# Kernel tuning notes

Hardware: AMD Instinct MI355X
Metric: run time of the kernel (lower is better)

The kernel has to match this reference:

```python
import jax, jax.numpy as jnp
import numpy as np

EPS = 1e-5
C = 128
B = 16384
SYMBIOTIC = 4.0
NUM_PARENTS = 16
CHILDREN_PER_PARENT = 7


def _inverse(v):
    # torch: sort -> rank -> reversed rank -> gather sorted values
    idx0 = np.argsort(v, kind='stable')
    value = v[idx0]
    idx1 = np.argsort(idx0, kind='stable')  # ranks
    idx2 = v.shape[0] - 1 - idx1
    return value[idx2]


def _build_stats():
    counts = np.floor(50000.0 * 0.97 ** np.arange(C)) + 1.0  # long-tailed
    N = counts.sum()
    weight = (N / counts).astype(np.float32)
    prior = np.eye(C, dtype=np.float32)
    for p in range(NUM_PARENTS):
        ch = NUM_PARENTS + CHILDREN_PER_PARENT * p + np.arange(CHILDREN_PER_PARENT)
        prior[p, ch] = 1.0
    prior_me = (prior == 0).astype(np.float32)          # 1 - prior, keep only exact 1s
    prior_ms = prior - np.eye(C, dtype=np.float32)      # prior (0/1) minus eye
    v1_sig = np.log(N / counts - 1.0 + EPS).astype(np.float32)
    v2_sig = _inverse(v1_sig).astype(np.float32)
    v1_sm = np.log(counts / N + EPS).astype(np.float32)
    v2_sm = _inverse(v1_sm).astype(np.float32)
    return weight, prior_me, prior_ms, v1_sig, v2_sig, v1_sm, v2_sm


def setup_inputs() -> dict:
    key = jax.random.key(0)
    k1, k2 = jax.random.split(key)
    weight, prior_me, prior_ms, v1s, v2s, v1m, v2m = _build_stats()
    logits = 0.5 * jax.random.normal(k1, (12, B, C), dtype=jnp.float32)
    target = (jax.random.uniform(k2, (B, C)) < 0.1).astype(jnp.float32)
    return {
        'logits': logits, 'target': target,
        'weight': jnp.asarray(weight),
        'prior_me': jnp.asarray(prior_me), 'prior_ms': jnp.asarray(prior_ms),
        'v1_sigmoid': jnp.asarray(v1s), 'v2_sigmoid': jnp.asarray(v2s),
        'v1_softmax': jnp.asarray(v1m), 'v2_softmax': jnp.asarray(v2m),
    }


def reference(logits, target, weight, prior_me, prior_ms,
              v1_sigmoid, v2_sigmoid, v1_softmax, v2_softmax):
    zero = jnp.zeros_like(v1_sigmoid)
    # experts 0-5: sigmoid variants (long-tailed / balanced / inversed, twice)
    sig_shift = jnp.stack([zero, v1_sigmoid, v1_sigmoid - v2_sigmoid] * 2)  # [6,C]
    a_sig = jax.nn.sigmoid(logits[:6] - sig_shift[:, None, :])
    # experts 6-11: local-softmax variants
    sm_shift = jnp.stack([zero, v1_softmax, v1_softmax - v2_softmax] * 2)   # [6,C]
    e = jnp.exp(logits[6:] + sm_shift[:, None, :])                          # [6,B,C]
    denom = jnp.einsum('ebc,cd->ebd', e, prior_me) + e
    a_sm = e / (denom + EPS)
    acti = jnp.clip(jnp.concatenate([a_sig, a_sm], axis=0), EPS, 1.0 - EPS)  # [12,B,C]
    # weighted BCE per expert, summed
    bce = -weight * (target * jnp.log(acti) + (1.0 - target) * jnp.log(1.0 - acti))
    loss = jnp.sum(jnp.mean(bce, axis=(1, 2)))
    # symbiotic regularizer on experts 3,4,5,9,10,11
    row_sum = jnp.sum(prior_ms, axis=1)                 # [C]
    n_nz = jnp.sum(row_sum > 0).astype(acti.dtype)
    bsz = acti.shape[1]

    def symb(a):  # a: [B,C] activated logits
        def step(acc, xs):
            mask_row, parent = xs                       # [C], [B]
            term = jnp.log1p(jnp.exp(a - parent[:, None]))  # [B,C]
            rs = jnp.sum(mask_row)
            contrib = jnp.where(rs > 0, jnp.sum(term * mask_row) / (bsz * rs), 0.0)
            return acc + contrib, None
        total, _ = jax.lax.scan(step, jnp.float32(0.0), (prior_ms, a.T))
        return total / n_nz

    reg = jax.vmap(symb)(acti[jnp.array([3, 4, 5, 9, 10, 11])])
    return loss + SYMBIOTIC * jnp.sum(reg)
```

## Files before the change

### kernel.cpp

```cpp
#include <hip/hip_runtime.h>
#include <math.h>

#define CC 128
#define BB 16384
#define MEPS 1e-5f
#define NBLK 2048


__device__ __forceinline__ float softplus1(float d) {
    const float u = d * d;
    float p = fmaf(u, 3.4722222e-4f, -5.2083333e-3f);
    p = fmaf(u, p, 0.125f);
    return fmaf(u, p, fmaf(d, 0.5f, 0.69314718f));
}

__global__ __launch_bounds__(256, 6) void mel_main(
    const float* __restrict__ logits, const float* __restrict__ target,
    const float* __restrict__ weight,
    const float* __restrict__ v1s, const float* __restrict__ v2s,
    const float* __restrict__ v1m, const float* __restrict__ v2m,
    float* __restrict__ partial)
{
    const int lane = threadIdx.x & 63;
    const int wib  = threadIdx.x >> 6;
    const int wave = blockIdx.x * 4 + wib;
    const int r    = lane >> 5;
    const int c    = lane & 31;
    const int row  = wave * 2 + r;
    const size_t ro = (size_t)row * CC;

    const float4 wt4 = ((const float4*)weight)[c];
    const float4 s1v = ((const float4*)v1s)[c];
    const float4 s2v = ((const float4*)v2s)[c];
    const float4 m1v = ((const float4*)v1m)[c];
    const float4 m2v = ((const float4*)v2m)[c];
    const float4 tv  = ((const float4*)(target + ro))[c];

    const float wt[4] = {wt4.x, wt4.y, wt4.z, wt4.w};
    const float s1[4] = {s1v.x, s1v.y, s1v.z, s1v.w};
    const float sd[4] = {s1v.x - s2v.x, s1v.y - s2v.y, s1v.z - s2v.z, s1v.w - s2v.w};
    const float m1[4] = {m1v.x, m1v.y, m1v.z, m1v.w};
    const float md[4] = {m1v.x - m2v.x, m1v.y - m2v.y, m1v.z - m2v.z, m1v.w - m2v.w};
    const bool  tb[4] = {tv.x > 0.5f, tv.y > 0.5f, tv.z > 0.5f, tv.w > 0.5f};

    const float childf = (c >= 4) ? 1.f : 0.f;
    int pofs[4];
    #pragma unroll
    for (int k = 0; k < 4; ++k) {
        const int ch = 4 * c + k;
        pofs[k] = (ch >= 16) ? (ch - 16) / 7 : 0;
    }

    __shared__ float lds[4][2][16];
    float* Lp = &lds[wib][r][0];

    const float* pp = logits + ro;
    float4 cur = ((const float4*)pp)[c];
    float accP = 0.f;
    float accS = 0.f;

    #pragma unroll 1
    for (int e = 0; e < 12; ++e) {
        float4 nxt = cur;
        if (e < 11) nxt = ((const float4*)(pp + (size_t)BB * CC))[c];
        pp += (size_t)BB * CC;
        const int si = e % 3;
        const float x[4] = {cur.x, cur.y, cur.z, cur.w};

        if (e < 6) {
            float a[4];
            #pragma unroll
            for (int k = 0; k < 4; ++k) {
                const float sh = (si == 0) ? 0.f : ((si == 1) ? s1[k] : sd[k]);
                const float z  = x[k] - sh;
                const float ex = __expf(-z);
                const float sp = __logf(1.f + ex);
                accP = fmaf(wt[k], sp + (tb[k] ? 0.f : z), accP);
                a[k] = __builtin_amdgcn_rcpf(1.f + ex);
            }
            if (e >= 3) {
                if (c < 4) *(float4*)(Lp + 4 * c) = make_float4(a[0], a[1], a[2], a[3]);
                #pragma unroll
                for (int k = 0; k < 4; ++k)
                    accS = fmaf(childf, softplus1(a[k] - Lp[pofs[k]]), accS);
            }
        } else {
            float ek[4];
            float S = 0.f;
            #pragma unroll
            for (int k = 0; k < 4; ++k) {
                const float sh = (si == 0) ? 0.f : ((si == 1) ? m1[k] : md[k]);
                ek[k] = __expf(x[k] + sh);
                S += ek[k];
            }
            #pragma unroll
            for (int off = 16; off > 0; off >>= 1)
                S += __shfl_xor(S, off, 64);
            const float Sj = S + MEPS;
            if (c < 4) *(float4*)(Lp + 4 * c) = make_float4(ek[0], ek[1], ek[2], ek[3]);
            const float rS = __builtin_amdgcn_rcpf(Sj);
            #pragma unroll
            for (int k = 0; k < 4; ++k) {
                const float ep  = Lp[pofs[k]];
                const float den = Sj - childf * ep;
                float a = ek[k] * __builtin_amdgcn_rcpf(den);
                a = fminf(fmaxf(a, MEPS), 1.f - MEPS);
                const float arg = tb[k] ? a : 1.f - a;
                accP = fmaf(wt[k], -__logf(arg), accP);
                if (e >= 9)
                    accS = fmaf(childf, softplus1(a - ep * rS), accS);
            }
        }
        cur = nxt;
    }

    float val = accP * (1.f / ((float)BB * (float)CC))
              + accS * (4.f / (112.f * (float)BB));

    #pragma unroll
    for (int off = 32; off > 0; off >>= 1)
        val += __shfl_xor(val, off, 64);

    __shared__ float sdata[4];
    if (lane == 0) sdata[wib] = val;
    __syncthreads();
    if (threadIdx.x == 0)
        partial[blockIdx.x] = (sdata[0] + sdata[1]) + (sdata[2] + sdata[3]);
}

__global__ __launch_bounds__(256) void mel_reduce(
    const float* __restrict__ partial, float* __restrict__ out)
{
    float v = 0.f;
    #pragma unroll
    for (int i = 0; i < NBLK / 256; ++i)
        v += partial[threadIdx.x + i * 256];
    #pragma unroll
    for (int off = 32; off > 0; off >>= 1)
        v += __shfl_xor(v, off, 64);
    __shared__ float s[4];
    const int lane = threadIdx.x & 63, wib = threadIdx.x >> 6;
    if (lane == 0) s[wib] = v;
    __syncthreads();
    if (threadIdx.x == 0) out[0] = (s[0] + s[1]) + (s[2] + s[3]);
}

extern "C" void kernel_launch(void* const* d_in, const int* in_sizes, int n_in,
                              void* d_out, int out_size, void* d_ws, size_t ws_size,
                              hipStream_t stream) {
    const float* logits = (const float*)d_in[0];
    const float* target = (const float*)d_in[1];
    const float* weight = (const float*)d_in[2];
    const float* v1s = (const float*)d_in[5];
    const float* v2s = (const float*)d_in[6];
    const float* v1m = (const float*)d_in[7];
    const float* v2m = (const float*)d_in[8];
    float* partial = (float*)d_ws;
    float* out = (float*)d_out;

    mel_main<<<NBLK, 256, 0, stream>>>(logits, target, weight,
                                       v1s, v2s, v1m, v2m, partial);
    mel_reduce<<<1, 256, 0, stream>>>(partial, out);
}
```

Measured before the change: 168.2 us.

## Process two rows per lane with two-deep prefetch and native exp2/log2 math

Halves the grid so each lane handles two rows, looping 24 times over experts and prefetching two iterations ahead, which keeps more loads in flight per wave. It also rewrites the math to use native exp2/log2 with the LOG2E/LN2 factors folded into the constants, turns the target branch into arithmetic, computes the sigmoid reciprocal only when the regularizer needs it, and replaces shuffle reductions with DPP/swizzle row sums. The risks are register pressure under the lower occupancy bound and fewer blocks to spread across the GPU.

Result: no change. 166.6 us (-1.0%).

```diff
diff --git a/kernel.cpp b/kernel.cpp
--- a/kernel.cpp
+++ b/kernel.cpp
@@ -4,7 +4,10 @@
 #define CC 128
 #define BB 16384
 #define MEPS 1e-5f
-#define NBLK 2048
+#define NBLK 1024
+#define EXPSTR ((size_t)BB * (size_t)CC)
+#define LOG2E 1.44269504f
+#define LN2   0.69314718f
 
 
 __device__ __forceinline__ float softplus1(float d) {
@@ -14,7 +17,22 @@
     return fmaf(u, p, fmaf(d, 0.5f, 0.69314718f));
 }
 
-__global__ __launch_bounds__(256, 6) void mel_main(
+template <int CTRL>
+__device__ __forceinline__ float dpp_addstep(float v) {
+    const int o = __builtin_amdgcn_update_dpp(0, __float_as_int(v), CTRL, 0xF, 0xF, true);
+    return v + __int_as_float(o);
+}
+
+__device__ __forceinline__ float rowsum32(float v) {
+    v += __int_as_float(__builtin_amdgcn_ds_swizzle(__float_as_int(v), 0x401F));
+    v = dpp_addstep<0x140>(v);
+    v = dpp_addstep<0x141>(v);
+    v = dpp_addstep<0x4E>(v);
+    v = dpp_addstep<0xB1>(v);
+    return v;
+}
+
+__global__ __launch_bounds__(256, 4) void mel_main(
     const float* __restrict__ logits, const float* __restrict__ target,
     const float* __restrict__ weight,
     const float* __restrict__ v1s, const float* __restrict__ v2s,
@@ -26,22 +44,30 @@
     const int wave = blockIdx.x * 4 + wib;
     const int r    = lane >> 5;
     const int c    = lane & 31;
-    const int row  = wave * 2 + r;
-    const size_t ro = (size_t)row * CC;
+    const size_t ro0 = (size_t)(wave * 2 + r) * CC;
+    const size_t ro1 = ro0 + (size_t)8192 * CC;
 
     const float4 wt4 = ((const float4*)weight)[c];
     const float4 s1v = ((const float4*)v1s)[c];
     const float4 s2v = ((const float4*)v2s)[c];
     const float4 m1v = ((const float4*)v1m)[c];
     const float4 m2v = ((const float4*)v2m)[c];
-    const float4 tv  = ((const float4*)(target + ro))[c];
-
-    const float wt[4] = {wt4.x, wt4.y, wt4.z, wt4.w};
-    const float s1[4] = {s1v.x, s1v.y, s1v.z, s1v.w};
-    const float sd[4] = {s1v.x - s2v.x, s1v.y - s2v.y, s1v.z - s2v.z, s1v.w - s2v.w};
-    const float m1[4] = {m1v.x, m1v.y, m1v.z, m1v.w};
-    const float md[4] = {m1v.x - m2v.x, m1v.y - m2v.y, m1v.z - m2v.z, m1v.w - m2v.w};
-    const bool  tb[4] = {tv.x > 0.5f, tv.y > 0.5f, tv.z > 0.5f, tv.w > 0.5f};
+    const float4 tA  = ((const float4*)(target + ro0))[c];
+    const float4 tB  = ((const float4*)(target + ro1))[c];
+
+    const float wl[4]  = {wt4.x * LN2, wt4.y * LN2, wt4.z * LN2, wt4.w * LN2};
+    const float s1[4]  = {s1v.x, s1v.y, s1v.z, s1v.w};
+    const float sd[4]  = {s1v.x - s2v.x, s1v.y - s2v.y, s1v.z - s2v.z, s1v.w - s2v.w};
+    const float m1l[4] = {m1v.x * LOG2E, m1v.y * LOG2E, m1v.z * LOG2E, m1v.w * LOG2E};
+    const float mdl[4] = {(m1v.x - m2v.x) * LOG2E, (m1v.y - m2v.y) * LOG2E,
+                          (m1v.z - m2v.z) * LOG2E, (m1v.w - m2v.w) * LOG2E};
+    const float t0Bv[4] = {tB.x > 0.5f ? 0.f : 1.f, tB.y > 0.5f ? 0.f : 1.f,
+                           tB.z > 0.5f ? 0.f : 1.f, tB.w > 0.5f ? 0.f : 1.f};
+    const float wzBv[4] = {wt4.x * t0Bv[0], wt4.y * t0Bv[1],
+                           wt4.z * t0Bv[2], wt4.w * t0Bv[3]};
+    float t0[4] = {tA.x > 0.5f ? 0.f : 1.f, tA.y > 0.5f ? 0.f : 1.f,
+                   tA.z > 0.5f ? 0.f : 1.f, tA.w > 0.5f ? 0.f : 1.f};
+    float wz[4] = {wt4.x * t0[0], wt4.y * t0[1], wt4.z * t0[2], wt4.w * t0[3]};
 
     const float childf = (c >= 4) ? 1.f : 0.f;
     int pofs[4];
@@ -54,31 +80,38 @@
     __shared__ float lds[4][2][16];
     float* Lp = &lds[wib][r][0];
 
-    const float* pp = logits + ro;
-    float4 cur = ((const float4*)pp)[c];
+    const float* pA = logits + ro0;
+    const float* pB = logits + ro1;
+    float4 cur = ((const float4*)pA)[c];
+    float4 b1  = ((const float4*)(pA + EXPSTR))[c];
+    const float* ppf = pA + 2 * EXPSTR;
+
     float accP = 0.f;
     float accS = 0.f;
+    int e = 0, si = 0;
 
     #pragma unroll 1
-    for (int e = 0; e < 12; ++e) {
-        float4 nxt = cur;
-        if (e < 11) nxt = ((const float4*)(pp + (size_t)BB * CC))[c];
-        pp += (size_t)BB * CC;
-        const int si = e % 3;
+    for (int i = 0; i < 24; ++i) {
+        float4 nxt = b1;
+        if (i < 22) nxt = ((const float4*)ppf)[c];
+        ppf = (i == 9) ? pB : (ppf + EXPSTR);
+
         const float x[4] = {cur.x, cur.y, cur.z, cur.w};
-
         if (e < 6) {
-            float a[4];
+            float q[4], z[4];
             #pragma unroll
             for (int k = 0; k < 4; ++k) {
                 const float sh = (si == 0) ? 0.f : ((si == 1) ? s1[k] : sd[k]);
-                const float z  = x[k] - sh;
-                const float ex = __expf(-z);
-                const float sp = __logf(1.f + ex);
-                accP = fmaf(wt[k], sp + (tb[k] ? 0.f : z), accP);
-                a[k] = __builtin_amdgcn_rcpf(1.f + ex);
+                z[k] = x[k] - sh;
+                const float ex = __builtin_amdgcn_exp2f(z[k] * -LOG2E);
+                q[k] = 1.f + ex;
+                accP = fmaf(wl[k], __builtin_amdgcn_logf(q[k]), accP);
+                accP = fmaf(wz[k], z[k], accP);
             }
             if (e >= 3) {
+                float a[4];
+                #pragma unroll
+                for (int k = 0; k < 4; ++k) a[k] = __builtin_amdgcn_rcpf(q[k]);
                 if (c < 4) *(float4*)(Lp + 4 * c) = make_float4(a[0], a[1], a[2], a[3]);
                 #pragma unroll
                 for (int k = 0; k < 4; ++k)
@@ -89,29 +122,34 @@
             float S = 0.f;
             #pragma unroll
             for (int k = 0; k < 4; ++k) {
-                const float sh = (si == 0) ? 0.f : ((si == 1) ? m1[k] : md[k]);
-                ek[k] = __expf(x[k] + sh);
+                const float shl = (si == 0) ? 0.f : ((si == 1) ? m1l[k] : mdl[k]);
+                ek[k] = __builtin_amdgcn_exp2f(fmaf(x[k], LOG2E, shl));
                 S += ek[k];
             }
-            #pragma unroll
-            for (int off = 16; off > 0; off >>= 1)
-                S += __shfl_xor(S, off, 64);
-            const float Sj = S + MEPS;
             if (c < 4) *(float4*)(Lp + 4 * c) = make_float4(ek[0], ek[1], ek[2], ek[3]);
+            const float Sj = rowsum32(S) + MEPS;
             const float rS = __builtin_amdgcn_rcpf(Sj);
             #pragma unroll
             for (int k = 0; k < 4; ++k) {
                 const float ep  = Lp[pofs[k]];
-                const float den = Sj - childf * ep;
+                const float den = fmaf(childf, -ep, Sj);
                 float a = ek[k] * __builtin_amdgcn_rcpf(den);
                 a = fminf(fmaxf(a, MEPS), 1.f - MEPS);
-                const float arg = tb[k] ? a : 1.f - a;
-                accP = fmaf(wt[k], -__logf(arg), accP);
+                const float arg = fmaf(t0[k], fmaf(-2.f, a, 1.f), a);
+                accP = fmaf(wl[k], -__builtin_amdgcn_logf(arg), accP);
                 if (e >= 9)
-                    accS = fmaf(childf, softplus1(a - ep * rS), accS);
+                    accS = fmaf(childf, softplus1(fmaf(ep, -rS, a)), accS);
             }
         }
-        cur = nxt;
+
+        cur = b1; b1 = nxt;
+        ++e; ++si;
+        if (si == 3) si = 0;
+        if (e == 12) {
+            e = 0;
+            #pragma unroll
+            for (int k = 0; k < 4; ++k) { t0[k] = t0Bv[k]; wz[k] = wzBv[k]; }
+        }
     }
 
     float val = accP * (1.f / ((float)BB * (float)CC))
```
